# Optimization experiments

Hardware: AMD Instinct MI355X
Metric: run time of the kernel (lower is better)

The kernel has to match this reference:

```python
import jax, jax.numpy as jnp
import numpy as np

N, E, G = 100000, 500000, 1000


def _gat(h_in, src, dst, W, a_s, a_d, b, n):
    # PyG GATConv, heads=1, concat=True, negative_slope=0.2, self-loops already in src/dst
    h = h_in @ W.T                                  # [N, out]
    alpha_src = h @ a_s                             # [N]
    alpha_dst = h @ a_d                             # [N]
    e = jax.nn.leaky_relu(alpha_src[src] + alpha_dst[dst], 0.2)  # [E']
    m = jax.ops.segment_max(e, dst, num_segments=n)
    ex = jnp.exp(e - m[dst])
    den = jax.ops.segment_sum(ex, dst, num_segments=n)
    alpha = ex / den[dst]                           # segment softmax over incoming edges
    out = jax.ops.segment_sum(h[src] * alpha[:, None], dst, num_segments=n)
    return out + b


def _forward(x, edge_index, batch, w1, b1, w2, b2, w3, b3,
             g1w, g1as, g1ad, g1b, g2w, g2as, g2ad, g2b,
             g3w, g3as, g3ad, g3b, g4w, g4as, g4ad, g4b,
             g5w, g5as, g5ad, g5b, lw, lb):
    n = x.shape[0]
    h = jax.nn.relu(x @ w1.T + b1)
    h = jax.nn.relu(h @ w2.T + b2)
    h = jax.nn.relu(h @ w3.T + b3)
    loops = jnp.arange(n)
    src = jnp.concatenate([edge_index[0], loops])   # add self-loops
    dst = jnp.concatenate([edge_index[1], loops])
    h = jax.nn.relu(_gat(h, src, dst, g1w, g1as, g1ad, g1b, n))
    h = jax.nn.relu(_gat(h, src, dst, g2w, g2as, g2ad, g2b, n))
    h = jax.nn.relu(_gat(h, src, dst, g3w, g3as, g3ad, g3b, n))
    h = jax.nn.relu(_gat(h, src, dst, g4w, g4as, g4ad, g4b, n))
    h = jax.nn.relu(_gat(h, src, dst, g5w, g5as, g5ad, g5b, n))
    sums = jax.ops.segment_sum(h, batch, num_segments=G)            # [G,32]
    cnt = jax.ops.segment_sum(jnp.ones((n,), h.dtype), batch, num_segments=G)
    mean = sums / jnp.maximum(cnt, 1.0)[:, None]
    return jax.nn.sigmoid(mean @ lw.T + lb)         # [G,1]


def setup_inputs() -> dict:
    key = jax.random.key(0)
    ks = jax.random.split(key, 24)

    def lin(k, o, i):
        k1, k2 = jax.random.split(k)
        s = 1.0 / np.sqrt(i)
        return (jax.random.uniform(k1, (o, i), jnp.float32, -s, s),
                jax.random.uniform(k2, (o,), jnp.float32, -s, s))

    def gat_p(k, i, o):
        k1, k2, k3 = jax.random.split(k, 3)
        s = 1.0 / np.sqrt(i)
        W = jax.random.uniform(k1, (o, i), jnp.float32, -s, s)
        a_s = jax.random.normal(k2, (o,), jnp.float32) / np.sqrt(o)
        a_d = jax.random.normal(k3, (o,), jnp.float32) / np.sqrt(o)
        return W, a_s, a_d, jnp.zeros((o,), jnp.float32)

    inp = {}
    inp['x'] = jax.random.normal(ks[0], (N, 1), jnp.float32)
    inp['edge_index'] = jax.random.randint(ks[1], (2, E), 0, N)
    inp['batch'] = jnp.sort(jax.random.randint(ks[2], (N,), 0, G))
    inp['w1'], inp['b1'] = lin(ks[3], 16, 1)
    inp['w2'], inp['b2'] = lin(ks[4], 32, 16)
    inp['w3'], inp['b3'] = lin(ks[5], 64, 32)
    dims = [(64, 128), (128, 256), (256, 128), (128, 64), (64, 32)]
    for j, (i, o) in enumerate(dims, start=1):
        W, a_s, a_d, b = gat_p(ks[5 + j], i, o)
        inp[f'g{j}w'], inp[f'g{j}as'], inp[f'g{j}ad'], inp[f'g{j}b'] = W, a_s, a_d, b
    inp['lw'], inp['lb'] = lin(ks[12], 1, 32)
    return inp


def reference(x, edge_index, batch, w1, b1, w2, b2, w3, b3,
              g1w, g1as, g1ad, g1b, g2w, g2as, g2ad, g2b,
              g3w, g3as, g3ad, g3b, g4w, g4as, g4ad, g4b,
              g5w, g5as, g5ad, g5b, lw, lb):
    return _forward(x, edge_index, batch, w1, b1, w2, b2, w3, b3,
                    g1w, g1as, g1ad, g1b, g2w, g2as, g2ad, g2b,
                    g3w, g3as, g3ad, g3b, g4w, g4as, g4ad, g4b,
                    g5w, g5as, g5ad, g5b, lw, lb)
```

## Files before the change

### kernel.cpp

```cpp
#include <hip/hip_runtime.h>
#include <math.h>

typedef __attribute__((ext_vector_type(8))) __bf16 bf16x8;
typedef __attribute__((ext_vector_type(4))) float f32x4;

__device__ inline unsigned short f2bf(float f) {
    unsigned int i = __float_as_uint(f);
    unsigned int r = i + 0x7fffu + ((i >> 16) & 1u);
    return (unsigned short)(r >> 16);
}
__device__ inline float bf2f(unsigned short u) {
    return __uint_as_float(((unsigned int)u) << 16);
}

__global__ __launch_bounds__(256) void mlp_kernel(
    const float* __restrict__ x,
    const float* __restrict__ w1, const float* __restrict__ b1,
    const float* __restrict__ w2, const float* __restrict__ b2,
    const float* __restrict__ w3, const float* __restrict__ b3,
    unsigned short* __restrict__ h0, int n,
    const float* __restrict__ g0,
    const float* __restrict__ as1, const float* __restrict__ ad1,
    float* __restrict__ s1out, float* __restrict__ d1out) {
    int tid = threadIdx.x;
    __shared__ float4 sw1q[4], sb1q[4];
    __shared__ float4 sw2q[128];
    __shared__ float4 sw3q[512];
    __shared__ float2 psd1[64];
    __shared__ float sb2l[32], sb3l[64];
    __shared__ float pres[4][64], predu[4][64];
    {
        int ii = tid & 63, ch = tid >> 6;
        const float* gp = g0 + (size_t)(ch * 32) * 64 + ii;
        float s = 0.f, d = 0.f;
#pragma unroll 4
        for (int o = 0; o < 32; o++) {
            float w = gp[o * 64];
            s += as1[ch * 32 + o] * w;
            d += ad1[ch * 32 + o] * w;
        }
        pres[ch][ii] = s;
        predu[ch][ii] = d;
    }
    if (tid < 4) { sw1q[tid] = ((const float4*)w1)[tid]; sb1q[tid] = ((const float4*)b1)[tid]; }
    if (tid >= 32 && tid < 64) sb2l[tid - 32] = b2[tid - 32];
    if (tid >= 64 && tid < 128) sb3l[tid - 64] = b3[tid - 64];
    for (int i = tid; i < 128; i += 256) sw2q[i] = ((const float4*)w2)[i];
    for (int i = tid; i < 512; i += 256) sw3q[i] = ((const float4*)w3)[i];
    __syncthreads();
    if (tid < 64) {
        psd1[tid] = make_float2(pres[0][tid] + pres[1][tid] + pres[2][tid] + pres[3][tid],
                                predu[0][tid] + predu[1][tid] + predu[2][tid] + predu[3][tid]);
    }
    __syncthreads();
    int node = blockIdx.x * 256 + tid;
    if (node >= n) return;
    float xv = x[node];
    float t1[16], t2[32];
#pragma unroll
    for (int q = 0; q < 4; q++) {
        float4 wv = sw1q[q], bv = sb1q[q];
        t1[q * 4 + 0] = fmaxf(wv.x * xv + bv.x, 0.f);
        t1[q * 4 + 1] = fmaxf(wv.y * xv + bv.y, 0.f);
        t1[q * 4 + 2] = fmaxf(wv.z * xv + bv.z, 0.f);
        t1[q * 4 + 3] = fmaxf(wv.w * xv + bv.w, 0.f);
    }
#pragma unroll
    for (int o = 0; o < 32; o++) {
        float a = sb2l[o];
#pragma unroll
        for (int q = 0; q < 4; q++) {
            float4 wv = sw2q[o * 4 + q];
            a += wv.x * t1[q * 4] + wv.y * t1[q * 4 + 1] + wv.z * t1[q * 4 + 2] +
                 wv.w * t1[q * 4 + 3];
        }
        t2[o] = fmaxf(a, 0.f);
    }
    float sdot = 0.f, ddot = 0.f;
    uint4* gp = (uint4*)(h0 + (size_t)node * 64);
#pragma unroll
    for (int c = 0; c < 8; c++) {
        unsigned int wvec[4];
#pragma unroll
        for (int p = 0; p < 4; p++) {
            int o = c * 8 + p * 2;
            float a0 = sb3l[o], a1 = sb3l[o + 1];
#pragma unroll
            for (int q = 0; q < 8; q++) {
                float4 wa = sw3q[o * 8 + q];
                float4 wb = sw3q[(o + 1) * 8 + q];
                a0 += wa.x * t2[q * 4] + wa.y * t2[q * 4 + 1] + wa.z * t2[q * 4 + 2] +
                      wa.w * t2[q * 4 + 3];
                a1 += wb.x * t2[q * 4] + wb.y * t2[q * 4 + 1] + wb.z * t2[q * 4 + 2] +
                      wb.w * t2[q * 4 + 3];
            }
            float r0 = fmaxf(a0, 0.f), r1 = fmaxf(a1, 0.f);
            float2 q0 = psd1[o], q1 = psd1[o + 1];
            sdot += r0 * q0.x + r1 * q1.x;
            ddot += r0 * q0.y + r1 * q1.y;
            wvec[p] = (unsigned)f2bf(r0) | ((unsigned)f2bf(r1) << 16);
        }
        gp[c] = make_uint4(wvec[0], wvec[1], wvec[2], wvec[3]);
    }
    s1out[node] = sdot;
    d1out[node] = ddot;
}

__global__ __launch_bounds__(256) void misc_kernel(
    const float* __restrict__ g0, const float* __restrict__ g1, const float* __restrict__ g2,
    const float* __restrict__ g3, const float* __restrict__ g4,
    unsigned short* __restrict__ wbAll,
    const int* __restrict__ batch, int* __restrict__ gstart, int G, int n,
    const int* __restrict__ dst, int* __restrict__ deg, int E,
    int f2bfB, int gsB, int histB,
    const float* __restrict__ as2, const float* __restrict__ ad2,
    float* __restrict__ pv2) {
    int b = blockIdx.x;
    int tid = threadIdx.x;
    if (b < f2bfB) {
        int i = b * 256 + tid;
        float v;
        if (i < 8192) v = g0[i];
        else if (i < 40960) v = g1[i - 8192];
        else if (i < 73728) v = g2[i - 40960];
        else if (i < 81920) v = g3[i - 73728];
        else if (i < 83968) v = g4[i - 81920];
        else return;
        wbAll[i] = f2bf(v);
    } else if (b < f2bfB + gsB) {
        int g = (b - f2bfB) * 256 + tid;
        if (g > G) return;
        if (g == G) { gstart[G] = n; return; }
        int lo = 0, hi = n;
        while (lo < hi) {
            int mid = (lo + hi) >> 1;
            if (batch[mid] < g) lo = mid + 1;
            else hi = mid;
        }
        gstart[g] = lo;
    } else if (b < f2bfB + gsB + histB) {
        int e = (b - f2bfB - gsB) * 256 + tid;
        if (e >= E) return;
        atomicAdd(&deg[dst[e]], 1);
    } else {
        if (tid < 128) {
            float s = 0.f;
            for (int o = 0; o < 256; o++) s += as2[o] * g1[o * 128 + tid];
            pv2[tid] = s;
        } else {
            int c = tid - 128;
            float s = 0.f;
            for (int o = 0; o < 256; o++) s += ad2[o] * g1[o * 128 + c];
            pv2[128 + c] = s;
        }
    }
}

template <int BN, int EPI>
__global__ __launch_bounds__(256) void gemm_mfma(
    const unsigned short* __restrict__ A, const unsigned short* __restrict__ Wb,
    unsigned short* __restrict__ Cb,
    const float* __restrict__ avs, const float* __restrict__ avd,
    float* __restrict__ as_, float* __restrict__ ad_,
    const float* __restrict__ bias, int n, int K, int O) {
    constexpr int SN = BN / 32;
    __shared__ unsigned short As[128][72];
    __shared__ unsigned short Ws[BN][72];
    int tid = threadIdx.x;
    int row0 = blockIdx.x * 128, col0 = blockIdx.y * BN;
    int w = tid >> 6, lane = tid & 63;
    int wr = w >> 1, wc = w & 1;
    int quad = lane >> 4, l15 = lane & 15;
    f32x4 acc[4][SN];
#pragma unroll
    for (int mi = 0; mi < 4; mi++)
#pragma unroll
        for (int ni = 0; ni < SN; ni++) acc[mi][ni] = (f32x4){0.f, 0.f, 0.f, 0.f};

    for (int k0 = 0; k0 < K; k0 += 64) {
#pragma unroll
        for (int i = tid; i < 1024; i += 256) {
            int r = i >> 3, c8 = i & 7;
            int gr = row0 + r;
            uint4 v = make_uint4(0u, 0u, 0u, 0u);
            if (gr < n) v = *(const uint4*)(A + (size_t)gr * K + k0 + c8 * 8);
            *(uint4*)&As[r][c8 * 8] = v;
        }
#pragma unroll
        for (int i = tid; i < BN * 8; i += 256) {
            int r = i >> 3, c8 = i & 7;
            uint4 v = *(const uint4*)(Wb + (size_t)(col0 + r) * K + k0 + c8 * 8);
            *(uint4*)&Ws[r][c8 * 8] = v;
        }
        __syncthreads();
#pragma unroll
        for (int kk = 0; kk < 64; kk += 32) {
            bf16x8 bfr[SN];
#pragma unroll
            for (int ni = 0; ni < SN; ni++)
                bfr[ni] = *(const bf16x8*)&Ws[wc * (BN / 2) + ni * 16 + l15][kk + quad * 8];
#pragma unroll
            for (int mi = 0; mi < 4; mi++) {
                bf16x8 afr = *(const bf16x8*)&As[wr * 64 + mi * 16 + l15][kk + quad * 8];
#pragma unroll
                for (int ni = 0; ni < SN; ni++)
                    acc[mi][ni] = __builtin_amdgcn_mfma_f32_16x16x32_bf16(afr, bfr[ni],
                                                                          acc[mi][ni], 0, 0, 0);
            }
        }
        __syncthreads();
    }
    float avsv[SN], avdv[SN], bv[SN];
    int gc[SN];
#pragma unroll
    for (int ni = 0; ni < SN; ni++) {
        gc[ni] = col0 + wc * (BN / 2) + ni * 16 + l15;
        if constexpr (EPI != 2) {
            avsv[ni] = avs[gc[ni]];
            avdv[ni] = avd[gc[ni]];
        }
        if constexpr (EPI >= 1) bv[ni] = bias[gc[ni]];
    }
#pragma unroll
    for (int mi = 0; mi < 4; mi++) {
        int gm0 = row0 + wr * 64 + mi * 16 + quad * 4;
        float ps[4] = {0.f, 0.f, 0.f, 0.f}, pd[4] = {0.f, 0.f, 0.f, 0.f};
#pragma unroll
        for (int ni = 0; ni < SN; ni++) {
#pragma unroll
            for (int r = 0; r < 4; r++) {
                float d = acc[mi][ni][r];
                if constexpr (EPI >= 1) d = fmaxf(d + bv[ni], 0.f);
                int gm = gm0 + r;
                if (gm < n) Cb[(size_t)gm * O + gc[ni]] = f2bf(d);
                if constexpr (EPI != 2) {
                    ps[r] += d * avsv[ni];
                    pd[r] += d * avdv[ni];
                }
            }
        }
        if constexpr (EPI != 2) {
#pragma unroll
            for (int r = 0; r < 4; r++) {
#pragma unroll
                for (int m = 1; m <= 8; m <<= 1) {
                    ps[r] += __shfl_xor(ps[r], m);
                    pd[r] += __shfl_xor(pd[r], m);
                }
            }
            if (l15 == 0) {
#pragma unroll
                for (int r = 0; r < 4; r++) {
                    int gm = gm0 + r;
                    if (gm < n) {
                        atomicAdd(&as_[gm], ps[r]);
                        atomicAdd(&ad_[gm], pd[r]);
                    }
                }
            }
        }
    }
}

__global__ void scan_block_sums(const int* __restrict__ deg, int* __restrict__ bsums, int n) {
    __shared__ int sdata[256];
    int tid = threadIdx.x;
    int base = blockIdx.x * 1024 + tid * 4;
    int s = 0;
    for (int i = 0; i < 4; i++) {
        int g = base + i;
        if (g < n) s += deg[g] + 1;
    }
    sdata[tid] = s;
    __syncthreads();
    for (int off = 128; off > 0; off >>= 1) {
        if (tid < off) sdata[tid] += sdata[tid + off];
        __syncthreads();
    }
    if (tid == 0) bsums[blockIdx.x] = sdata[0];
}

__global__ void scan_write(const int* __restrict__ deg, const int* __restrict__ bsums,
                           int* __restrict__ rowptr, int* __restrict__ cursor,
                           int* __restrict__ esrc, int n, int nb) {
    __shared__ int sdata[256];
    int tid = threadIdx.x;
    sdata[tid] = (tid < blockIdx.x && tid < nb) ? bsums[tid] : 0;
    __syncthreads();
    for (int off = 128; off > 0; off >>= 1) {
        if (tid < off) sdata[tid] += sdata[tid + off];
        __syncthreads();
    }
    int base = sdata[0];
    __syncthreads();
    int gbase = blockIdx.x * 1024 + tid * 4;
    int v[4];
    int s = 0;
    for (int i = 0; i < 4; i++) {
        int g = gbase + i;
        v[i] = (g < n) ? deg[g] + 1 : 0;
        s += v[i];
    }
    sdata[tid] = s;
    __syncthreads();
    for (int off = 1; off < 256; off <<= 1) {
        int t = (tid >= off) ? sdata[tid - off] : 0;
        __syncthreads();
        sdata[tid] += t;
        __syncthreads();
    }
    int excl = sdata[tid] - s + base;
    for (int i = 0; i < 4; i++) {
        int g = gbase + i;
        if (g < n) {
            rowptr[g] = excl;
            esrc[excl] = g;
            cursor[g] = excl + 1;
        }
        excl += v[i];
    }
    if (blockIdx.x == gridDim.x - 1 && tid == 255) rowptr[n] = base + sdata[255];
}

__global__ void scatter_kernel(const int* __restrict__ esrc_in, const int* __restrict__ edst_in,
                               int* __restrict__ cursor, int* __restrict__ esrc, int E) {
    int e = blockIdx.x * 256 + threadIdx.x;
    if (e >= E) return;
    int pos = atomicAdd(&cursor[edst_in[e]], 1);
    esrc[pos] = esrc_in[e];
}

template <int O, bool BIASRELU>
__global__ __launch_bounds__(256) void gat_aggregate(
    const unsigned short* __restrict__ hl, const float* __restrict__ as_,
    const float* __restrict__ ad_, const int* __restrict__ rowptr,
    const int* __restrict__ esrc, const float* __restrict__ bias,
    unsigned short* __restrict__ hout, int n, float* __restrict__ zeroBuf, int zeroCnt) {
    int gtid = blockIdx.x * 256 + threadIdx.x;
    if (gtid < zeroCnt) zeroBuf[gtid] = 0.f;
    constexpr int C8 = O / 8;
    constexpr int EPP = 16 / C8;
    int tid = threadIdx.x;
    int v = blockIdx.x * 16 + (tid >> 4);
    int l = tid & 15;
    int gbase = tid & 48;
    if (v >= n) return;
    int beg = rowptr[v], end = rowptr[v + 1];
    int deg = end - beg;
    float adv = ad_[v];
    int sub = l / C8;
    int c = l % C8;
    float acc[8] = {0.f, 0.f, 0.f, 0.f, 0.f, 0.f, 0.f, 0.f};
    if (deg <= 16) {
        int sreg = v;
        float e = -1e30f;
        if (l < deg) {
            sreg = esrc[beg + l];
            float t = as_[sreg] + adv;
            e = (t > 0.f) ? t : 0.2f * t;
        }
        float m = e;
#pragma unroll
        for (int o = 8; o > 0; o >>= 1) m = fmaxf(m, __shfl_xor(m, o));
        float ex = (l < deg) ? __expf(e - m) : 0.f;
        float sum = ex;
#pragma unroll
        for (int o = 8; o > 0; o >>= 1) sum += __shfl_xor(sum, o);
        float alpha_r = ex / sum;
        for (int j0 = 0; j0 < deg; j0 += EPP) {
            int idx = j0 + sub;
            int cidx = (idx < deg) ? idx : 0;
            float alpha = __shfl(alpha_r, gbase + cidx);
            int s2 = __shfl(sreg, gbase + cidx);
            if (idx >= deg) alpha = 0.f;
            uint4 raw = ((const uint4*)(hl + (size_t)s2 * O))[c];
            acc[0] += alpha * __uint_as_float(raw.x << 16);
            acc[1] += alpha * __uint_as_float(raw.x & 0xffff0000u);
            acc[2] += alpha * __uint_as_float(raw.y << 16);
            acc[3] += alpha * __uint_as_float(raw.y & 0xffff0000u);
            acc[4] += alpha * __uint_as_float(raw.z << 16);
            acc[5] += alpha * __uint_as_float(raw.z & 0xffff0000u);
            acc[6] += alpha * __uint_as_float(raw.w << 16);
            acc[7] += alpha * __uint_as_float(raw.w & 0xffff0000u);
        }
    } else {
        float mymax = -1e30f;
        for (int j = beg + l; j < end; j += 16) {
            float e = as_[esrc[j]] + adv;
            e = (e > 0.f) ? e : 0.2f * e;
            mymax = fmaxf(mymax, e);
        }
#pragma unroll
        for (int o = 8; o > 0; o >>= 1) mymax = fmaxf(mymax, __shfl_xor(mymax, o));
        float mysum = 0.f;
        for (int j = beg + l; j < end; j += 16) {
            float e = as_[esrc[j]] + adv;
            e = (e > 0.f) ? e : 0.2f * e;
            mysum += __expf(e - mymax);
        }
#pragma unroll
        for (int o = 8; o > 0; o >>= 1) mysum += __shfl_xor(mysum, o);
        float invden = 1.f / mysum;
        for (int j0 = beg; j0 < end; j0 += EPP) {
            int j = j0 + sub;
            bool valid = j < end;
            int s = valid ? esrc[j] : v;
            float e = as_[s] + adv;
            e = (e > 0.f) ? e : 0.2f * e;
            float alpha = valid ? __expf(e - mymax) * invden : 0.f;
            uint4 raw = ((const uint4*)(hl + (size_t)s * O))[c];
            acc[0] += alpha * __uint_as_float(raw.x << 16);
            acc[1] += alpha * __uint_as_float(raw.x & 0xffff0000u);
            acc[2] += alpha * __uint_as_float(raw.y << 16);
            acc[3] += alpha * __uint_as_float(raw.y & 0xffff0000u);
            acc[4] += alpha * __uint_as_float(raw.z << 16);
            acc[5] += alpha * __uint_as_float(raw.z & 0xffff0000u);
            acc[6] += alpha * __uint_as_float(raw.w << 16);
            acc[7] += alpha * __uint_as_float(raw.w & 0xffff0000u);
        }
    }
#pragma unroll
    for (int o = C8; o < 16; o <<= 1)
#pragma unroll
        for (int k = 0; k < 8; k++) acc[k] += __shfl_xor(acc[k], o);
    if (l < C8) {
        unsigned short ov[8];
#pragma unroll
        for (int k = 0; k < 8; k++) {
            float val = acc[k];
            if constexpr (BIASRELU) val = fmaxf(val + bias[c * 8 + k], 0.f);
            ov[k] = f2bf(val);
        }
        uint4 packed;
        packed.x = (unsigned)ov[0] | ((unsigned)ov[1] << 16);
        packed.y = (unsigned)ov[2] | ((unsigned)ov[3] << 16);
        packed.z = (unsigned)ov[4] | ((unsigned)ov[5] << 16);
        packed.w = (unsigned)ov[6] | ((unsigned)ov[7] << 16);
        ((uint4*)(hout + (size_t)v * O))[c] = packed;
    }
}

__global__ __launch_bounds__(256) void pool_final_kernel(
    const unsigned short* __restrict__ h, const int* __restrict__ start,
    const float* __restrict__ lw, const float* __restrict__ lb,
    float* __restrict__ out, int G) {
    __shared__ float red[8][33];
    int g = blockIdx.x;
    if (g >= G) return;
    int beg = start[g], end = start[g + 1];
    int tid = threadIdx.x;
    int nodeLane = tid >> 5, f = tid & 31;
    float acc = 0.f;
    for (int v = beg + nodeLane; v < end; v += 8)
        acc += bf2f(h[(size_t)v * 32 + f]);
    red[nodeLane][f] = acc;
    __syncthreads();
    if (tid < 32) {
        float s = 0.f;
#pragma unroll
        for (int i = 0; i < 8; i++) s += red[i][f];
        float inv = 1.f / fmaxf((float)(end - beg), 1.f);
        float val = s * inv * lw[f];
#pragma unroll
        for (int o = 16; o > 0; o >>= 1) val += __shfl_xor(val, o);
        if (f == 0) out[g] = 1.f / (1.f + __expf(-(val + lb[0])));
    }
}

extern "C" void kernel_launch(void* const* d_in, const int* in_sizes, int n_in,
                              void* d_out, int out_size, void* d_ws, size_t ws_size,
                              hipStream_t stream) {
    const float* x = (const float*)d_in[0];
    const int* ei = (const int*)d_in[1];
    const int* batch = (const int*)d_in[2];
    const float* w1 = (const float*)d_in[3];
    const float* b1 = (const float*)d_in[4];
    const float* w2 = (const float*)d_in[5];
    const float* b2 = (const float*)d_in[6];
    const float* w3 = (const float*)d_in[7];
    const float* b3 = (const float*)d_in[8];
    const float* gw[5];
    const float* gas[5];
    const float* gad[5];
    const float* gb[5];
    for (int l = 0; l < 5; l++) {
        gw[l] = (const float*)d_in[9 + l * 4 + 0];
        gas[l] = (const float*)d_in[9 + l * 4 + 1];
        gad[l] = (const float*)d_in[9 + l * 4 + 2];
        gb[l] = (const float*)d_in[9 + l * 4 + 3];
    }
    const float* lw = (const float*)d_in[29];
    const float* lb = (const float*)d_in[30];
    float* out = (float*)d_out;

    int N = in_sizes[0];
    int E = in_sizes[1] / 2;
    int G = out_size;
    int Etot = E + N;

    char* ws = (char*)d_ws;
    size_t off = 0;
    auto alloc = [&](size_t bytes) -> void* {
        void* p = ws + off;
        off = (off + bytes + 255) & ~(size_t)255;
        return p;
    };
    unsigned short* actA = (unsigned short*)alloc((size_t)N * 256 * 2);
    unsigned short* actB = (unsigned short*)alloc((size_t)N * 256 * 2);
    char* zblock = (char*)alloc((size_t)N * 20);
    float* sd2 = (float*)zblock;
    float* sd3 = sd2 + (size_t)N * 2;
    int* deg = (int*)(zblock + (size_t)N * 16);
    float* sd1 = (float*)alloc((size_t)N * 2 * 4);
    float* pv2 = (float*)alloc(256 * 4);
    int* rowptr = (int*)alloc((size_t)(N + 1) * 4);
    int* cursor = (int*)alloc((size_t)(N + 1) * 4);
    int* esrc = (int*)alloc((size_t)Etot * 4);
    int* bsums = (int*)alloc(4096);
    int* gstart = (int*)alloc((size_t)(G + 1) * 4);
    unsigned short* wbAll = (unsigned short*)alloc((size_t)83968 * 2);
    const int woff[5] = {0, 8192, 40960, 73728, 81920};
    unsigned short* wb[5];
    for (int l = 0; l < 5; l++) wb[l] = wbAll + woff[l];
    (void)ws_size;
    (void)n_in;

    hipMemsetAsync(zblock, 0, (size_t)N * 20, stream);

    int f2bfB = (83968 + 255) / 256;
    int gsB = (G + 1 + 255) / 256;
    int histB = (E + 255) / 256;
    misc_kernel<<<f2bfB + gsB + histB + 1, 256, 0, stream>>>(
        gw[0], gw[1], gw[2], gw[3], gw[4], wbAll, batch, gstart, G, N, ei + E, deg, E,
        f2bfB, gsB, histB, gas[1], gad[1], pv2);

    mlp_kernel<<<(N + 255) / 256, 256, 0, stream>>>(x, w1, b1, w2, b2, w3, b3, actA, N,
                                                    gw[0], gas[0], gad[0], sd1, sd1 + N);

    int nb = (N + 1023) / 1024;
    scan_block_sums<<<nb, 256, 0, stream>>>(deg, bsums, N);
    scan_write<<<nb, 256, 0, stream>>>(deg, bsums, rowptr, cursor, esrc, N, nb);
    scatter_kernel<<<(E + 255) / 256, 256, 0, stream>>>(ei, ei + E, cursor, esrc, E);

    int aggBlocks = (N + 15) / 16;
    int gx = (N + 127) / 128;

    gat_aggregate<64, false><<<aggBlocks, 256, 0, stream>>>(
        actA, sd1, sd1 + N, rowptr, esrc, nullptr, actB, N, nullptr, 0);
    {
        dim3 grid(gx, 2);
        gemm_mfma<64, 1><<<grid, 256, 0, stream>>>(actB, wb[0], actA, pv2, pv2 + 128, sd2,
                                                   sd2 + N, gb[0], N, 64, 128);
    }

    gat_aggregate<128, false><<<aggBlocks, 256, 0, stream>>>(
        actA, sd2, sd2 + N, rowptr, esrc, nullptr, actB, N, sd1, 2 * N);
    {
        dim3 grid(gx, 4);
        gemm_mfma<64, 2><<<grid, 256, 0, stream>>>(actB, wb[1], actA, nullptr, nullptr,
                                                   nullptr, nullptr, gb[1], N, 128, 256);
    }

    {
        dim3 grid(gx, 2);
        gemm_mfma<64, 0><<<grid, 256, 0, stream>>>(actA, wb[2], actB, gas[2], gad[2], sd3,
                                                   sd3 + N, nullptr, N, 256, 128);
    }
    gat_aggregate<128, true><<<aggBlocks, 256, 0, stream>>>(
        actB, sd3, sd3 + N, rowptr, esrc, gb[2], actA, N, sd2, 2 * N);

    {
        dim3 grid(gx, 1);
        gemm_mfma<64, 0><<<grid, 256, 0, stream>>>(actA, wb[3], actB, gas[3], gad[3], sd1,
                                                   sd1 + N, nullptr, N, 128, 64);
    }
    gat_aggregate<64, true><<<aggBlocks, 256, 0, stream>>>(
        actB, sd1, sd1 + N, rowptr, esrc, gb[3], actA, N, nullptr, 0);

    {
        dim3 grid(gx, 1);
        gemm_mfma<32, 0><<<grid, 256, 0, stream>>>(actA, wb[4], actB, gas[4], gad[4], sd2,
                                                   sd2 + N, nullptr, N, 64, 32);
    }
    gat_aggregate<32, true><<<aggBlocks, 256, 0, stream>>>(
        actB, sd2, sd2 + N, rowptr, esrc, gb[4], actA, N, nullptr, 0);

    pool_final_kernel<<<G, 256, 0, stream>>>(actA, gstart, lw, lb, out, G);
}
```

Measured before the change: 468.1 us.

## Sort nodes by degree bucket to balance work in GAT aggregation

Builds a per-degree histogram (capped at 31) during the scan, computes bucket offsets, and writes a permutation that orders nodes by in-degree. Each aggregate kernel then processes nodes in this permuted order, so the 16-lane groups in a wavefront handle nodes of similar degree and divergence is reduced. In exchange it adds a kernel launch, global atomics, and an extra indirection. Output writes become scattered and lose locality, since consecutive groups no longer handle consecutive node ids.

Result: slower. 549.7 us (+17.4%).

```diff
diff --git a/kernel.cpp b/kernel.cpp
--- a/kernel.cpp
+++ b/kernel.cpp
@@ -262,14 +262,22 @@
     }
 }
 
-__global__ void scan_block_sums(const int* __restrict__ deg, int* __restrict__ bsums, int n) {
+__global__ void scan_block_sums(const int* __restrict__ deg, int* __restrict__ bsums,
+                                int* __restrict__ bhist, int n) {
     __shared__ int sdata[256];
+    __shared__ int lh[32];
     int tid = threadIdx.x;
+    if (tid < 32) lh[tid] = 0;
+    __syncthreads();
     int base = blockIdx.x * 1024 + tid * 4;
     int s = 0;
     for (int i = 0; i < 4; i++) {
         int g = base + i;
-        if (g < n) s += deg[g] + 1;
+        if (g < n) {
+            int dv = deg[g] + 1;
+            s += dv;
+            atomicAdd(&lh[min(dv, 31)], 1);
+        }
     }
     sdata[tid] = s;
     __syncthreads();
@@ -278,14 +286,26 @@
         __syncthreads();
     }
     if (tid == 0) bsums[blockIdx.x] = sdata[0];
+    if (tid < 32 && lh[tid]) atomicAdd(&bhist[tid], lh[tid]);
+}
+
+__global__ void bucket_scan(const int* __restrict__ bhist, int* __restrict__ bcur) {
+    if (threadIdx.x == 0) {
+        int acc = 0;
+        for (int b = 0; b < 32; b++) { bcur[b] = acc; acc += bhist[b]; }
+    }
 }
 
 __global__ void scan_write(const int* __restrict__ deg, const int* __restrict__ bsums,
                            int* __restrict__ rowptr, int* __restrict__ cursor,
-                           int* __restrict__ esrc, int n, int nb) {
+                           int* __restrict__ esrc, int* __restrict__ bcur,
+                           int* __restrict__ perm, int n, int nb) {
     __shared__ int sdata[256];
+    __shared__ int lh[32];
+    __shared__ int gb[32];
     int tid = threadIdx.x;
     sdata[tid] = (tid < blockIdx.x && tid < nb) ? bsums[tid] : 0;
+    if (tid < 32) lh[tid] = 0;
     __syncthreads();
     for (int off = 128; off > 0; off >>= 1) {
         if (tid < off) sdata[tid] += sdata[tid + off];
@@ -294,15 +314,17 @@
     int base = sdata[0];
     __syncthreads();
     int gbase = blockIdx.x * 1024 + tid * 4;
-    int v[4];
+    int v[4], lrank[4];
     int s = 0;
     for (int i = 0; i < 4; i++) {
         int g = gbase + i;
         v[i] = (g < n) ? deg[g] + 1 : 0;
         s += v[i];
+        if (g < n) lrank[i] = atomicAdd(&lh[min(v[i], 31)], 1);
     }
     sdata[tid] = s;
     __syncthreads();
+    if (tid < 32 && lh[tid]) gb[tid] = atomicAdd(&bcur[tid], lh[tid]);
     for (int off = 1; off < 256; off <<= 1) {
         int t = (tid >= off) ? sdata[tid - off] : 0;
         __syncthreads();
@@ -316,6 +338,7 @@
             rowptr[g] = excl;
             esrc[excl] = g;
             cursor[g] = excl + 1;
+            perm[gb[min(v[i], 31)] + lrank[i]] = g;
         }
         excl += v[i];
     }
@@ -334,17 +357,19 @@
 __global__ __launch_bounds__(256) void gat_aggregate(
     const unsigned short* __restrict__ hl, const float* __restrict__ as_,
     const float* __restrict__ ad_, const int* __restrict__ rowptr,
-    const int* __restrict__ esrc, const float* __restrict__ bias,
+    const int* __restrict__ esrc, const int* __restrict__ perm,
+    const float* __restrict__ bias,
     unsigned short* __restrict__ hout, int n, float* __restrict__ zeroBuf, int zeroCnt) {
     int gtid = blockIdx.x * 256 + threadIdx.x;
     if (gtid < zeroCnt) zeroBuf[gtid] = 0.f;
     constexpr int C8 = O / 8;
     constexpr int EPP = 16 / C8;
     int tid = threadIdx.x;
-    int v = blockIdx.x * 16 + (tid >> 4);
+    int idx = blockIdx.x * 16 + (tid >> 4);
     int l = tid & 15;
     int gbase = tid & 48;
-    if (v >= n) return;
+    if (idx >= n) return;
+    int v = perm[idx];
     int beg = rowptr[v], end = rowptr[v + 1];
     int deg = end - beg;
     float adv = ad_[v];
@@ -368,11 +393,11 @@
         for (int o = 8; o > 0; o >>= 1) sum += __shfl_xor(sum, o);
         float alpha_r = ex / sum;
         for (int j0 = 0; j0 < deg; j0 += EPP) {
-            int idx = j0 + sub;
-            int cidx = (idx < deg) ? idx : 0;
+            int idx2 = j0 + sub;
+            int cidx = (idx2 < deg) ? idx2 : 0;
             float alpha = __shfl(alpha_r, gbase + cidx);
             int s2 = __shfl(sreg, gbase + cidx);
-            if (idx >= deg) alpha = 0.f;
+            if (idx2 >= deg) alpha = 0.f;
             uint4 raw = ((const uint4*)(hl + (size_t)s2 * O))[c];
             acc[0] += alpha * __uint_as_float(raw.x << 16);
             acc[1] += alpha * __uint_as_float(raw.x & 0xffff0000u);
@@ -507,14 +532,17 @@
     };
     unsigned short* actA = (unsigned short*)alloc((size_t)N * 256 * 2);
     unsigned short* actB = (unsigned short*)alloc((size_t)N * 256 * 2);
-    char* zblock = (char*)alloc((size_t)N * 20);
+    char* zblock = (char*)alloc((size_t)N * 20 + 256);
     float* sd2 = (float*)zblock;
     float* sd3 = sd2 + (size_t)N * 2;
     int* deg = (int*)(zblock + (size_t)N * 16);
+    int* bhist = (int*)(zblock + (size_t)N * 20);
+    int* bcur = bhist + 32;
     float* sd1 = (float*)alloc((size_t)N * 2 * 4);
     float* pv2 = (float*)alloc(256 * 4);
     int* rowptr = (int*)alloc((size_t)(N + 1) * 4);
     int* cursor = (int*)alloc((size_t)(N + 1) * 4);
+    int* perm = (int*)alloc((size_t)N * 4);
     int* esrc = (int*)alloc((size_t)Etot * 4);
     int* bsums = (int*)alloc(4096);
     int* gstart = (int*)alloc((size_t)(G + 1) * 4);
@@ -525,7 +553,7 @@
     (void)ws_size;
     (void)n_in;
 
-    hipMemsetAsync(zblock, 0, (size_t)N * 20, stream);
+    hipMemsetAsync(zblock, 0, (size_t)N * 20 + 256, stream);
 
     int f2bfB = (83968 + 255) / 256;
     int gsB = (G + 1 + 255) / 256;
@@ -538,15 +566,16 @@
                                                     gw[0], gas[0], gad[0], sd1, sd1 + N);
 
     int nb = (N + 1023) / 1024;
-    scan_block_sums<<<nb, 256, 0, stream>>>(deg, bsums, N);
-    scan_write<<<nb, 256, 0, stream>>>(deg, bsums, rowptr, cursor, esrc, N, nb);
+    scan_block_sums<<<nb, 256, 0, stream>>>(deg, bsums, bhist, N);
+    bucket_scan<<<1, 64, 0, stream>>>(bhist, bcur);
+    scan_write<<<nb, 256, 0, stream>>>(deg, bsums, rowptr, cursor, esrc, bcur, perm, N, nb);
     scatter_kernel<<<(E + 255) / 256, 256, 0, stream>>>(ei, ei + E, cursor, esrc, E);
 
     int aggBlocks = (N + 15) / 16;
     int gx = (N + 127) / 128;
 
     gat_aggregate<64, false><<<aggBlocks, 256, 0, stream>>>(
-        actA, sd1, sd1 + N, rowptr, esrc, nullptr, actB, N, nullptr, 0);
+        actA, sd1, sd1 + N, rowptr, esrc, perm, nullptr, actB, N, nullptr, 0);
     {
         dim3 grid(gx, 2);
         gemm_mfma<64, 1><<<grid, 256, 0, stream>>>(actB, wb[0], actA, pv2, pv2 + 128, sd2,
@@ -554,7 +583,7 @@
     }
 
     gat_aggregate<128, false><<<aggBlocks, 256, 0, stream>>>(
-        actA, sd2, sd2 + N, rowptr, esrc, nullptr, actB, N, sd1, 2 * N);
+        actA, sd2, sd2 + N, rowptr, esrc, perm, nullptr, actB, N, sd1, 2 * N);
     {
         dim3 grid(gx, 4);
         gemm_mfma<64, 2><<<grid, 256, 0, stream>>>(actB, wb[1], actA, nullptr, nullptr,
@@ -567,7 +596,7 @@
                                                    sd3 + N, nullptr, N, 256, 128);
     }
     gat_aggregate<128, true><<<aggBlocks, 256, 0, stream>>>(
-        actB, sd3, sd3 + N, rowptr, esrc, gb[2], actA, N, sd2, 2 * N);
+        actB, sd3, sd3 + N, rowptr, esrc, perm, gb[2], actA, N, sd2, 2 * N);
 
     {
         dim3 grid(gx, 1);
@@ -575,7 +604,7 @@
                                                    sd1 + N, nullptr, N, 128, 64);
     }
     gat_aggregate<64, true><<<aggBlocks, 256, 0, stream>>>(
-        actB, sd1, sd1 + N, rowptr, esrc, gb[3], actA, N, nullptr, 0);
+        actB, sd1, sd1 + N, rowptr, esrc, perm, gb[3], actA, N, nullptr, 0);
 
     {
         dim3 grid(gx, 1);
@@ -583,7 +612,7 @@
                                                    sd2 + N, nullptr, N, 64, 32);
     }
     gat_aggregate<32, true><<<aggBlocks, 256, 0, stream>>>(
-        actB, sd2, sd2 + N, rowptr, esrc, gb[4], actA, N, nullptr, 0);
+        actB, sd2, sd2 + N, rowptr, esrc, perm, gb[4], actA, N, nullptr, 0);
 
     pool_final_kernel<<<G, 256, 0, stream>>>(actA, gstart, lw, lb, out, G);
 }
```
